# Performance work log

Measured on AMD Instinct MI355X. Metric: run time of the kernel, lower is better.

The kernel has to match this reference:

```python
import jax, jax.numpy as jnp
import numpy as np

DIM = 1024
H = 16
DH = 64
INNER = H * DH
SCALE = DH ** -0.5


def setup_inputs() -> dict:
    key = jax.random.key(0)
    ks = jax.random.split(key, 6)
    B, L, R = 4, 4096, 512
    x = jax.random.normal(ks[0], (B, L, DIM), dtype=jnp.float32)
    context = jax.random.normal(ks[1], (B, R, DIM), dtype=jnp.float32)
    s = DIM ** -0.5
    Wq = jax.random.normal(ks[2], (DIM, INNER), dtype=jnp.float32) * s
    Wk = jax.random.normal(ks[3], (DIM, INNER), dtype=jnp.float32) * s
    Wv = jax.random.normal(ks[4], (DIM, INNER), dtype=jnp.float32) * s
    Wo = jax.random.normal(ks[5], (INNER, DIM), dtype=jnp.float32) * (INNER ** -0.5)
    return {"x": x, "context": context, "Wq": Wq, "Wk": Wk, "Wv": Wv, "Wo": Wo}


def reference(x, context, Wq, Wk, Wv, Wo):
    B, L, _ = x.shape
    R = context.shape[1]
    # project and split heads: (B, H, L/R, Dh)
    q = (x @ Wq).reshape(B, L, H, DH).transpose(0, 2, 1, 3)
    k = (context @ Wk).reshape(B, R, H, DH).transpose(0, 2, 1, 3)
    v = (context @ Wv).reshape(B, R, H, DH).transpose(0, 2, 1, 3)
    scores = jnp.einsum('bhld,bhrd->bhlr', q, k) * SCALE  # (B,H,L,R)
    attn = jax.nn.softmax(scores, axis=-1)
    out = jnp.einsum('bhlr,bhrd->bhld', attn, v)
    out = out.transpose(0, 2, 1, 3).reshape(B, L, INNER)
    return out @ Wo
```

## Files before the change

kernel.cpp:

```cpp
#include <hip/hip_runtime.h>
#include <hip/hip_bf16.h>

#define DIMC 1024
#define HEADS 16
#define DHEAD 64
#define LQ 4096
#define RK 512
#define BATCH 4

#define QSCALE 0.18033688011112042f

using bf16x8  = __attribute__((ext_vector_type(8))) __bf16;
using short4v = __attribute__((ext_vector_type(4))) short;
using f32x4   = __attribute__((ext_vector_type(4))) float;

__device__ inline ushort f2bf(float f) {
  __hip_bfloat16 h = __float2bfloat16(f);
  return *reinterpret_cast<ushort*>(&h);
}

__device__ inline float exp2_fast(float x) {
  float r; asm("v_exp_f32 %0, %1" : "=v"(r) : "v"(x)); return r;
}

__global__ __launch_bounds__(256) void prep(const float* __restrict__ x,
    const float* __restrict__ ctx, ushort* __restrict__ xb,
    ushort* __restrict__ ctxb,
    const float* __restrict__ W0, const float* __restrict__ W1,
    const float* __restrict__ W2, const float* __restrict__ W3,
    ushort* __restrict__ D0, ushort* __restrict__ D1,
    ushort* __restrict__ D2, ushort* __restrict__ D3) {
  __shared__ ushort tile[32][33];
  const int bid = blockIdx.x;
  if (bid < 9216) {
    size_t i = ((size_t)bid * 256 + threadIdx.x) * 8;
    const float* src; ushort* dst; size_t off;
    if (i < (size_t)16777216) { src = x; dst = xb; off = i; }
    else { src = ctx; dst = ctxb; off = i - 16777216; }
    float4 a = *(const float4*)(src + off);
    float4 b = *(const float4*)(src + off + 4);
    ushort u[8];
    u[0]=f2bf(a.x); u[1]=f2bf(a.y); u[2]=f2bf(a.z); u[3]=f2bf(a.w);
    u[4]=f2bf(b.x); u[5]=f2bf(b.y); u[6]=f2bf(b.z); u[7]=f2bf(b.w);
    *(uint4*)(dst + off) = *(const uint4*)u;
    return;
  }
  const int tb = bid - 9216;
  const int z = tb >> 10, rem = tb & 1023;
  const int bx = rem & 31, by = rem >> 5;
  const float* src = (z == 0) ? W0 : (z == 1) ? W1 : (z == 2) ? W2 : W3;
  ushort* dst = (z == 0) ? D0 : (z == 1) ? D1 : (z == 2) ? D2 : D3;
  const int tx = threadIdx.x & 31, ty = threadIdx.x >> 5;
  const int xg = bx * 32 + tx;
  #pragma unroll
  for (int j = 0; j < 32; j += 8)
    tile[ty + j][tx] = f2bf(src[(size_t)(by * 32 + ty + j) * DIMC + xg]);
  __syncthreads();
  const int xo = by * 32 + tx;
  #pragma unroll
  for (int j = 0; j < 32; j += 8)
    dst[(size_t)(bx * 32 + ty + j) * DIMC + xo] = tile[tx][ty + j];
}

__global__ __launch_bounds__(256, 4) void gemm_qkv(const ushort* __restrict__ xb,
    const ushort* __restrict__ ctxb, const ushort* __restrict__ WqT,
    const ushort* __restrict__ WkvT, ushort* __restrict__ Qw,
    ushort* __restrict__ Kw, ushort* __restrict__ Vt) {
  __shared__ ushort As[128 * 32];
  __shared__ ushort Bs[128 * 32];
  const int tid  = threadIdx.x;
  const int wave = tid >> 6, lane = tid & 63;
  const int lr = lane & 15, quad = lane >> 4;
  const ushort* A; const ushort* Bt; size_t m0, n0; int seg;
  if (blockIdx.y < 128) {
    int bid = blockIdx.y * 8 + blockIdx.x;
    int swz = (bid & 7) * 128 + (bid >> 3);
    m0 = (size_t)(swz >> 3) * 128;
    n0 = (size_t)(swz & 7) * 128;
    A = xb; Bt = WqT; seg = 0;
  } else {
    int bid = (blockIdx.y - 128) * 8 + blockIdx.x;
    int swz = (bid & 7) * 32 + (bid >> 3);
    m0 = (size_t)(swz >> 4) * 128;
    n0 = (size_t)(swz & 15) * 128;
    A = ctxb; Bt = WkvT; seg = 1;
  }
  const int wm = (wave >> 1) * 64, wn = (wave & 1) * 64;
  f32x4 acc[4][4] = {};
  for (int k0 = 0; k0 < DIMC; k0 += 32) {
    __syncthreads();
    #pragma unroll
    for (int t = 0; t < 2; ++t) {
      int c = (wave * 2 + t) * 64 + lane;
      int row = c >> 2, cc = c & 3;
      const ushort* ga = A  + (m0 + row) * DIMC + k0 + cc * 8;
      const ushort* gb = Bt + (n0 + row) * DIMC + k0 + cc * 8;
      __builtin_amdgcn_global_load_lds(
          (__attribute__((address_space(1))) void*)ga,
          (__attribute__((address_space(3))) void*)(As + (size_t)(wave * 2 + t) * 512),
          16, 0, 0);
      __builtin_amdgcn_global_load_lds(
          (__attribute__((address_space(1))) void*)gb,
          (__attribute__((address_space(3))) void*)(Bs + (size_t)(wave * 2 + t) * 512),
          16, 0, 0);
    }
    __syncthreads();
    bf16x8 af[4], bfr[4];
    #pragma unroll
    for (int mt = 0; mt < 4; ++mt)
      af[mt] = *(const bf16x8*)(As + (wm + mt * 16 + lr) * 32 + quad * 8);
    #pragma unroll
    for (int nt = 0; nt < 4; ++nt)
      bfr[nt] = *(const bf16x8*)(Bs + (wn + nt * 16 + lr) * 32 + quad * 8);
    #pragma unroll
    for (int mt = 0; mt < 4; ++mt)
      #pragma unroll
      for (int nt = 0; nt < 4; ++nt)
        acc[mt][nt] = __builtin_amdgcn_mfma_f32_16x16x32_bf16(
            af[mt], bfr[nt], acc[mt][nt], 0, 0, 0);
  }
  if (seg == 0) {
    #pragma unroll
    for (int mt = 0; mt < 4; ++mt)
      #pragma unroll
      for (int nt = 0; nt < 4; ++nt)
        #pragma unroll
        for (int j = 0; j < 4; ++j) {
          size_t m = m0 + wm + mt * 16 + quad * 4 + j;
          size_t n = n0 + wn + nt * 16 + lr;
          Qw[m * DIMC + n] = f2bf(acc[mt][nt][j] * QSCALE);
        }
  } else if (n0 < 1024) {
    #pragma unroll
    for (int mt = 0; mt < 4; ++mt)
      #pragma unroll
      for (int nt = 0; nt < 4; ++nt)
        #pragma unroll
        for (int j = 0; j < 4; ++j) {
          size_t m = m0 + wm + mt * 16 + quad * 4 + j;
          size_t n = n0 + wn + nt * 16 + lr;
          Kw[m * DIMC + n] = f2bf(acc[mt][nt][j]);
        }
  } else {
    #pragma unroll
    for (int mt = 0; mt < 4; ++mt)
      #pragma unroll
      for (int nt = 0; nt < 4; ++nt) {
        size_t m = m0 + wm + mt * 16 + quad * 4;
        int hcol = (int)(n0 + wn + nt * 16 + lr) - 1024;
        int h = hcol >> 6, dh = hcol & 63;
        int bb = (int)(m >> 9), r = (int)(m & 511);
        ushort o4[4];
        #pragma unroll
        for (int j = 0; j < 4; ++j) o4[j] = f2bf(acc[mt][nt][j]);
        *(ushort4*)(Vt + (((size_t)bb * HEADS + h) * 64 + dh) * RK + r) =
            *(const ushort4*)o4;
      }
  }
}

__global__ __launch_bounds__(256, 4) void gemm_bt(const ushort* __restrict__ A,
    const ushort* __restrict__ Bt, float* __restrict__ C32) {
  __shared__ ushort As[128 * 32];
  __shared__ ushort Bs[128 * 32];
  const int tid  = threadIdx.x;
  const int wave = tid >> 6, lane = tid & 63;
  const int lr = lane & 15, quad = lane >> 4;
  const int nbx = gridDim.x;
  const int bid = blockIdx.y * nbx + blockIdx.x;
  const int cpx = (nbx * gridDim.y) >> 3;
  const int swz = (bid & 7) * cpx + (bid >> 3);
  const int bx = swz % nbx, by = swz / nbx;
  const size_t m0 = (size_t)by * 128;
  const size_t n0 = (size_t)bx * 128;
  const int wm = (wave >> 1) * 64, wn = (wave & 1) * 64;
  f32x4 acc[4][4] = {};
  for (int k0 = 0; k0 < DIMC; k0 += 32) {
    __syncthreads();
    #pragma unroll
    for (int t = 0; t < 2; ++t) {
      int c = (wave * 2 + t) * 64 + lane;
      int row = c >> 2, cc = c & 3;
      const ushort* ga = A  + (m0 + row) * DIMC + k0 + cc * 8;
      const ushort* gb = Bt + (n0 + row) * DIMC + k0 + cc * 8;
      __builtin_amdgcn_global_load_lds(
          (__attribute__((address_space(1))) void*)ga,
          (__attribute__((address_space(3))) void*)(As + (size_t)(wave * 2 + t) * 512),
          16, 0, 0);
      __builtin_amdgcn_global_load_lds(
          (__attribute__((address_space(1))) void*)gb,
          (__attribute__((address_space(3))) void*)(Bs + (size_t)(wave * 2 + t) * 512),
          16, 0, 0);
    }
    __syncthreads();
    bf16x8 af[4], bfr[4];
    #pragma unroll
    for (int mt = 0; mt < 4; ++mt)
      af[mt] = *(const bf16x8*)(As + (wm + mt * 16 + lr) * 32 + quad * 8);
    #pragma unroll
    for (int nt = 0; nt < 4; ++nt)
      bfr[nt] = *(const bf16x8*)(Bs + (wn + nt * 16 + lr) * 32 + quad * 8);
    #pragma unroll
    for (int mt = 0; mt < 4; ++mt)
      #pragma unroll
      for (int nt = 0; nt < 4; ++nt)
        acc[mt][nt] = __builtin_amdgcn_mfma_f32_16x16x32_bf16(
            af[mt], bfr[nt], acc[mt][nt], 0, 0, 0);
  }
  #pragma unroll
  for (int mt = 0; mt < 4; ++mt)
    #pragma unroll
    for (int nt = 0; nt < 4; ++nt)
      #pragma unroll
      for (int j = 0; j < 4; ++j) {
        size_t m = m0 + wm + mt * 16 + quad * 4 + j;
        size_t n = n0 + wn + nt * 16 + lr;
        C32[m * DIMC + n] = acc[mt][nt][j];
      }
}

__global__ __launch_bounds__(256) void attn(ushort* __restrict__ QO,
    const ushort* __restrict__ K, const ushort* __restrict__ Vt) {
  __shared__ __align__(16) ushort Ks[128 * 64];
  __shared__ __align__(16) ushort Vs[64 * 128];
  const int tid  = threadIdx.x;
  const int wave = tid >> 6, lane = tid & 63;
  const int lr = lane & 15, quad = lane >> 4;
  const int b = blockIdx.z, h = blockIdx.y, qb = blockIdx.x;
  const int lsw = (lr & 7) << 3;

  bf16x8 bq[2];
  {
    size_t row = (size_t)b * LQ + qb * 64 + wave * 16 + lr;
    const ushort* qp = QO + row * DIMC + h * DHEAD + quad * 8;
    bq[0] = *(const bf16x8*)(qp);
    bq[1] = *(const bf16x8*)(qp + 32);
  }

  const int krow = tid >> 3, kcol = (tid & 7) * 8;
  const int vrow = tid >> 4, vcol = (tid & 15) * 8;
  const int kwsw = (krow & 7) << 3;
  const int vwsw = (vrow & 7) << 3;
  const ushort* Kbase = K  + ((size_t)b * RK) * DIMC + h * DHEAD;
  const ushort* Vbase = Vt + (((size_t)b * HEADS + h) * 64) * RK;

  uint4 kr0, kr1, kr2, kr3, vr0, vr1, vr2, vr3;
#define LOADK(rc_, i_) \
  (*(const uint4*)(Kbase + (size_t)((rc_) * 128 + (i_) * 32 + krow) * DIMC + kcol))
#define LOADV(rc_, i_) \
  (*(const uint4*)(Vbase + (size_t)((i_) * 16 + vrow) * RK + (rc_) * 128 + vcol))
#define ISSUE(rc_) do {                                      \
    kr0 = LOADK(rc_, 0); kr1 = LOADK(rc_, 1);                \
    kr2 = LOADK(rc_, 2); kr3 = LOADK(rc_, 3);                \
    vr0 = LOADV(rc_, 0); vr1 = LOADV(rc_, 1);                \
    vr2 = LOADV(rc_, 2); vr3 = LOADV(rc_, 3);                \
  } while (0)

  ISSUE(0);

  float mi = -1e30f, li = 0.f;
  f32x4 o[4] = {};

  for (int rc = 0; rc < 4; ++rc) {
    __syncthreads();
    *(uint4*)(Ks + ((((0 * 32 + krow) * 64) + kcol) ^ kwsw)) = kr0;
    *(uint4*)(Ks + ((((1 * 32 + krow) * 64) + kcol) ^ kwsw)) = kr1;
    *(uint4*)(Ks + ((((2 * 32 + krow) * 64) + kcol) ^ kwsw)) = kr2;
    *(uint4*)(Ks + ((((3 * 32 + krow) * 64) + kcol) ^ kwsw)) = kr3;
    *(uint4*)(Vs + ((((0 * 16 + vrow) * 128) + vcol) ^ vwsw)) = vr0;
    *(uint4*)(Vs + ((((1 * 16 + vrow) * 128) + vcol) ^ vwsw)) = vr1;
    *(uint4*)(Vs + ((((2 * 16 + vrow) * 128) + vcol) ^ vwsw)) = vr2;
    *(uint4*)(Vs + ((((3 * 16 + vrow) * 128) + vcol) ^ vwsw)) = vr3;
    __syncthreads();
    if (rc < 3) ISSUE(rc + 1);

    float s[8][4];
    __builtin_amdgcn_s_setprio(1);
    #pragma unroll
    for (int nt = 0; nt < 8; ++nt) {
      f32x4 acc = {};
      acc = __builtin_amdgcn_mfma_f32_16x16x32_bf16(
          *(const bf16x8*)(Ks + ((((nt * 16 + lr) * 64) + quad * 8) ^ lsw)),
          bq[0], acc, 0, 0, 0);
      acc = __builtin_amdgcn_mfma_f32_16x16x32_bf16(
          *(const bf16x8*)(Ks + ((((nt * 16 + lr) * 64) + quad * 8 + 32) ^ lsw)),
          bq[1], acc, 0, 0, 0);
      #pragma unroll
      for (int j = 0; j < 4; ++j) s[nt][j] = acc[j];
    }
    __builtin_amdgcn_s_setprio(0);

    float c0 = s[0][0], c1 = s[0][1], c2 = s[0][2], c3 = s[0][3];
    #pragma unroll
    for (int nt = 1; nt < 8; ++nt) {
      c0 = fmaxf(c0, s[nt][0]); c1 = fmaxf(c1, s[nt][1]);
      c2 = fmaxf(c2, s[nt][2]); c3 = fmaxf(c3, s[nt][3]);
    }
    float cm = fmaxf(fmaxf(c0, c1), fmaxf(c2, c3));
    cm = fmaxf(cm, __shfl_xor(cm, 16));
    cm = fmaxf(cm, __shfl_xor(cm, 32));

    if (!__all(cm - mi <= 8.f)) {
      float mnew = fmaxf(mi, cm);
      float alpha = exp2_fast(mi - mnew);
      mi = mnew;
      li *= alpha;
      float a_bc[4];
      #pragma unroll
      for (int j = 0; j < 4; ++j) a_bc[j] = __shfl(alpha, quad * 4 + j, 16);
      #pragma unroll
      for (int n2 = 0; n2 < 4; ++n2)
        #pragma unroll
        for (int j = 0; j < 4; ++j) o[n2][j] *= a_bc[j];
    }

    short4v pf[8];
    float r0 = 0.f, r1 = 0.f, r2 = 0.f, r3 = 0.f;
    #pragma unroll
    for (int nt = 0; nt < 8; ++nt) {
      float p0 = exp2_fast(s[nt][0] - mi);
      float p1 = exp2_fast(s[nt][1] - mi);
      float p2 = exp2_fast(s[nt][2] - mi);
      float p3 = exp2_fast(s[nt][3] - mi);
      r0 += p0; r1 += p1; r2 += p2; r3 += p3;
      pf[nt][0] = (short)f2bf(p0); pf[nt][1] = (short)f2bf(p1);
      pf[nt][2] = (short)f2bf(p2); pf[nt][3] = (short)f2bf(p3);
    }
    float rs = (r0 + r1) + (r2 + r3);
    rs += __shfl_xor(rs, 16);
    rs += __shfl_xor(rs, 32);
    li += rs;

    __builtin_amdgcn_s_setprio(1);
    #pragma unroll
    for (int kt = 0; kt < 8; ++kt)
      #pragma unroll
      for (int n2 = 0; n2 < 4; ++n2) {
        short4v bv = *(const short4v*)(
            Vs + ((((n2 * 16 + lr) * 128) + kt * 16 + quad * 4) ^ lsw));
        o[n2] = __builtin_amdgcn_mfma_f32_16x16x16bf16_1k(pf[kt], bv, o[n2], 0, 0, 0);
      }
    __builtin_amdgcn_s_setprio(0);
  }
#undef LOADK
#undef LOADV
#undef ISSUE

  float li_bc[4];
  #pragma unroll
  for (int j = 0; j < 4; ++j) li_bc[j] = __shfl(li, quad * 4 + j, 16);
  #pragma unroll
  for (int n2 = 0; n2 < 4; ++n2)
    #pragma unroll
    for (int j = 0; j < 4; ++j) {
      size_t row = (size_t)b * LQ + qb * 64 + wave * 16 + quad * 4 + j;
      QO[row * DIMC + h * DHEAD + n2 * 16 + lr] = f2bf(o[n2][j] / li_bc[j]);
    }
}

extern "C" void kernel_launch(void* const* d_in, const int* in_sizes, int n_in,
                              void* d_out, int out_size, void* d_ws, size_t ws_size,
                              hipStream_t stream) {
  const float* x   = (const float*)d_in[0];
  const float* ctx = (const float*)d_in[1];

  ushort* outs = (ushort*)d_out;
  ushort* xb   = outs;
  ushort* ctxb = outs + (size_t)16777216;
  ushort* WqT  = outs + (size_t)18874368;
  ushort* WkT  = outs + (size_t)19922944;
  ushort* WvT  = outs + (size_t)20971520;
  ushort* Kw   = outs + (size_t)22020096;
  ushort* Vt_g = outs + (size_t)24117248;

  ushort* ws  = (ushort*)d_ws;
  ushort* Qw  = ws;
  ushort* WoT = ws + (size_t)16384 * 1024;

  prep<<<13312, 256, 0, stream>>>(x, ctx, xb, ctxb,
      (const float*)d_in[2], (const float*)d_in[3], (const float*)d_in[4],
      (const float*)d_in[5], WqT, WkT, WvT, WoT);
  gemm_qkv<<<dim3(8, 160), 256, 0, stream>>>(xb, ctxb, WqT, WkT, Qw, Kw, Vt_g);
  attn<<<dim3(LQ / 64, HEADS, BATCH), 256, 0, stream>>>(Qw, Kw, Vt_g);
  gemm_bt<<<dim3(8, 128), 256, 0, stream>>>(Qw, WoT, (float*)d_out);
}
```

Before: 302.7 us.

## Double GEMM K-tile to 64 and XOR-swizzle LDS layout in projection GEMMs

Both projection GEMM kernels now stage a 64-wide K slice per iteration instead of 32, which halves the number of barrier pairs and load rounds per output tile. The LDS tiles use an XOR swizzle of 16-byte chunks by row, so the strided bf16x8 fragment reads spread across banks instead of conflicting. The cost is twice the shared memory per block (32 KB), which may reduce how many blocks fit per CU under the launch bound of 4.

Result: no change. 302.2 us (-0.1%).

```diff
diff --git a/kernel.cpp b/kernel.cpp
--- a/kernel.cpp
+++ b/kernel.cpp
@@ -66,8 +66,8 @@
     const ushort* __restrict__ ctxb, const ushort* __restrict__ WqT,
     const ushort* __restrict__ WkvT, ushort* __restrict__ Qw,
     ushort* __restrict__ Kw, ushort* __restrict__ Vt) {
-  __shared__ ushort As[128 * 32];
-  __shared__ ushort Bs[128 * 32];
+  __shared__ ushort As[128 * 64];
+  __shared__ ushort Bs[128 * 64];
   const int tid  = threadIdx.x;
   const int wave = tid >> 6, lane = tid & 63;
   const int lr = lane & 15, quad = lane >> 4;
@@ -86,38 +86,45 @@
     A = ctxb; Bt = WkvT; seg = 1;
   }
   const int wm = (wave >> 1) * 64, wn = (wave & 1) * 64;
+  const int rsw = lr & 7;
   f32x4 acc[4][4] = {};
-  for (int k0 = 0; k0 < DIMC; k0 += 32) {
-    __syncthreads();
-    #pragma unroll
-    for (int t = 0; t < 2; ++t) {
-      int c = (wave * 2 + t) * 64 + lane;
-      int row = c >> 2, cc = c & 3;
-      const ushort* ga = A  + (m0 + row) * DIMC + k0 + cc * 8;
-      const ushort* gb = Bt + (n0 + row) * DIMC + k0 + cc * 8;
+  for (int k0 = 0; k0 < DIMC; k0 += 64) {
+    __syncthreads();
+    #pragma unroll
+    for (int t = 0; t < 4; ++t) {
+      int c = (wave * 4 + t) * 64 + lane;
+      int row = c >> 3, cc = c & 7;
+      int col = (cc ^ (row & 7)) * 8;
+      const ushort* ga = A  + (m0 + row) * DIMC + k0 + col;
+      const ushort* gb = Bt + (n0 + row) * DIMC + k0 + col;
       __builtin_amdgcn_global_load_lds(
           (__attribute__((address_space(1))) void*)ga,
-          (__attribute__((address_space(3))) void*)(As + (size_t)(wave * 2 + t) * 512),
+          (__attribute__((address_space(3))) void*)(As + (size_t)(wave * 4 + t) * 512),
           16, 0, 0);
       __builtin_amdgcn_global_load_lds(
           (__attribute__((address_space(1))) void*)gb,
-          (__attribute__((address_space(3))) void*)(Bs + (size_t)(wave * 2 + t) * 512),
+          (__attribute__((address_space(3))) void*)(Bs + (size_t)(wave * 4 + t) * 512),
           16, 0, 0);
     }
     __syncthreads();
-    bf16x8 af[4], bfr[4];
-    #pragma unroll
-    for (int mt = 0; mt < 4; ++mt)
-      af[mt] = *(const bf16x8*)(As + (wm + mt * 16 + lr) * 32 + quad * 8);
-    #pragma unroll
-    for (int nt = 0; nt < 4; ++nt)
-      bfr[nt] = *(const bf16x8*)(Bs + (wn + nt * 16 + lr) * 32 + quad * 8);
-    #pragma unroll
-    for (int mt = 0; mt < 4; ++mt)
+    #pragma unroll
+    for (int ks = 0; ks < 2; ++ks) {
+      bf16x8 af[4], bfr[4];
+      #pragma unroll
+      for (int mt = 0; mt < 4; ++mt)
+        af[mt] = *(const bf16x8*)(As + (wm + mt * 16 + lr) * 64
+                                     + (((ks * 4 + quad) ^ rsw) * 8));
       #pragma unroll
       for (int nt = 0; nt < 4; ++nt)
-        acc[mt][nt] = __builtin_amdgcn_mfma_f32_16x16x32_bf16(
-            af[mt], bfr[nt], acc[mt][nt], 0, 0, 0);
+        bfr[nt] = *(const bf16x8*)(Bs + (wn + nt * 16 + lr) * 64
+                                      + (((ks * 4 + quad) ^ rsw) * 8));
+      #pragma unroll
+      for (int mt = 0; mt < 4; ++mt)
+        #pragma unroll
+        for (int nt = 0; nt < 4; ++nt)
+          acc[mt][nt] = __builtin_amdgcn_mfma_f32_16x16x32_bf16(
+              af[mt], bfr[nt], acc[mt][nt], 0, 0, 0);
+    }
   }
   if (seg == 0) {
     #pragma unroll
@@ -161,8 +168,8 @@
 
 __global__ __launch_bounds__(256, 4) void gemm_bt(const ushort* __restrict__ A,
     const ushort* __restrict__ Bt, float* __restrict__ C32) {
-  __shared__ ushort As[128 * 32];
-  __shared__ ushort Bs[128 * 32];
+  __shared__ ushort As[128 * 64];
+  __shared__ ushort Bs[128 * 64];
   const int tid  = threadIdx.x;
   const int wave = tid >> 6, lane = tid & 63;
   const int lr = lane & 15, quad = lane >> 4;
@@ -174,38 +181,45 @@
   const size_t m0 = (size_t)by * 128;
   const size_t n0 = (size_t)bx * 128;
   const int wm = (wave >> 1) * 64, wn = (wave & 1) * 64;
+  const int rsw = lr & 7;
   f32x4 acc[4][4] = {};
-  for (int k0 = 0; k0 < DIMC; k0 += 32) {
-    __syncthreads();
-    #pragma unroll
-    for (int t = 0; t < 2; ++t) {
-      int c = (wave * 2 + t) * 64 + lane;
-      int row = c >> 2, cc = c & 3;
-      const ushort* ga = A  + (m0 + row) * DIMC + k0 + cc * 8;
-      const ushort* gb = Bt + (n0 + row) * DIMC + k0 + cc * 8;
+  for (int k0 = 0; k0 < DIMC; k0 += 64) {
+    __syncthreads();
+    #pragma unroll
+    for (int t = 0; t < 4; ++t) {
+      int c = (wave * 4 + t) * 64 + lane;
+      int row = c >> 3, cc = c & 7;
+      int col = (cc ^ (row & 7)) * 8;
+      const ushort* ga = A  + (m0 + row) * DIMC + k0 + col;
+      const ushort* gb = Bt + (n0 + row) * DIMC + k0 + col;
       __builtin_amdgcn_global_load_lds(
           (__attribute__((address_space(1))) void*)ga,
-          (__attribute__((address_space(3))) void*)(As + (size_t)(wave * 2 + t) * 512),
+          (__attribute__((address_space(3))) void*)(As + (size_t)(wave * 4 + t) * 512),
           16, 0, 0);
       __builtin_amdgcn_global_load_lds(
           (__attribute__((address_space(1))) void*)gb,
-          (__attribute__((address_space(3))) void*)(Bs + (size_t)(wave * 2 + t) * 512),
+          (__attribute__((address_space(3))) void*)(Bs + (size_t)(wave * 4 + t) * 512),
           16, 0, 0);
     }
     __syncthreads();
-    bf16x8 af[4], bfr[4];
-    #pragma unroll
-    for (int mt = 0; mt < 4; ++mt)
-      af[mt] = *(const bf16x8*)(As + (wm + mt * 16 + lr) * 32 + quad * 8);
-    #pragma unroll
-    for (int nt = 0; nt < 4; ++nt)
-      bfr[nt] = *(const bf16x8*)(Bs + (wn + nt * 16 + lr) * 32 + quad * 8);
-    #pragma unroll
-    for (int mt = 0; mt < 4; ++mt)
+    #pragma unroll
+    for (int ks = 0; ks < 2; ++ks) {
+      bf16x8 af[4], bfr[4];
+      #pragma unroll
+      for (int mt = 0; mt < 4; ++mt)
+        af[mt] = *(const bf16x8*)(As + (wm + mt * 16 + lr) * 64
+                                     + (((ks * 4 + quad) ^ rsw) * 8));
       #pragma unroll
       for (int nt = 0; nt < 4; ++nt)
-        acc[mt][nt] = __builtin_amdgcn_mfma_f32_16x16x32_bf16(
-            af[mt], bfr[nt], acc[mt][nt], 0, 0, 0);
+        bfr[nt] = *(const bf16x8*)(Bs + (wn + nt * 16 + lr) * 64
+                                      + (((ks * 4 + quad) ^ rsw) * 8));
+      #pragma unroll
+      for (int mt = 0; mt < 4; ++mt)
+        #pragma unroll
+        for (int nt = 0; nt < 4; ++nt)
+          acc[mt][nt] = __builtin_amdgcn_mfma_f32_16x16x32_bf16(
+              af[mt], bfr[nt], acc[mt][nt], 0, 0, 0);
+    }
   }
   #pragma unroll
   for (int mt = 0; mt < 4; ++mt)
```
